# Performance work log

Hardware: AMD Instinct MI355X
Metric: run time of the kernel (lower is better)

The kernel has to match this reference:

```python
import jax, jax.numpy as jnp
import numpy as np

D_MODEL = 1024
NUM_PROTOTYPES = 1024
TOPK = 5
ALPHA = 0.1
EPS = 1e-12  # matches torch F.normalize default eps


def setup_inputs() -> dict:
    key = jax.random.key(0)
    kx, kp = jax.random.split(key)
    x = jax.random.normal(kx, (32, 2048, D_MODEL), dtype=jnp.float32)
    prototypes = jax.random.normal(kp, (NUM_PROTOTYPES, D_MODEL), dtype=jnp.float32)
    return {"x": x, "prototypes": prototypes}


def _l2_normalize(v, axis=-1):
    # torch F.normalize: v / max(||v||, eps)
    n = jnp.linalg.norm(v, axis=axis, keepdims=True)
    return v / jnp.maximum(n, EPS)


def reference(x, prototypes):
    # x: [B, L, D]; prototypes: [P, D]
    query = jnp.mean(x, axis=1)                       # [B, D] global pool
    query_n = _l2_normalize(query)                    # [B, D]
    proto_n = _l2_normalize(prototypes)               # [P, D]
    scores = jnp.einsum('bd,pd->bp', query_n, proto_n)  # [B, P] cosine sims
    topk_scores, topk_idx = jax.lax.top_k(scores, TOPK)  # [B, K]
    attn = jax.nn.softmax(topk_scores, axis=-1)       # [B, K]
    retrieved = prototypes[topk_idx]                  # [B, K, D] gather
    proto_agg = jnp.einsum('bk,bkd->bd', attn, retrieved)  # [B, D]
    out = x + ALPHA * proto_agg[:, None, :]           # broadcast residual add
    return out
```

## Files before the change

### kernel.cpp

```cpp
#include <hip/hip_runtime.h>
#include <math.h>

#define D_MODEL 1024
#define D4 256
#define SEQ 2048
#define BATCH 32
#define NUM_PROTO 1024
#define TOPK 5
#define ALPHA 0.1f
#define EPS 1e-12f
#define CHUNKS 64
#define CHUNK_ROWS (SEQ / CHUNKS)

typedef float f4v __attribute__((ext_vector_type(4)));

__device__ __forceinline__ float block_reduce_sum_256(float v) {
    __shared__ float red[4];
    for (int o = 32; o; o >>= 1) v += __shfl_down(v, o, 64);
    const int wave = threadIdx.x >> 6;
    const int lane = threadIdx.x & 63;
    __syncthreads();
    if (lane == 0) red[wave] = v;
    __syncthreads();
    return (red[0] + red[1]) + (red[2] + red[3]);
}

__global__ void mean_partial(const float* __restrict__ x, float* __restrict__ part) {
    const int blk = blockIdx.x;
    const int b = blk >> 6;
    const int c = blk & (CHUNKS - 1);
    const int t = threadIdx.x;
    const float4* xb = (const float4*)(x + (size_t)b * SEQ * D_MODEL
                                         + (size_t)c * CHUNK_ROWS * D_MODEL);
    float4 acc = {0.f, 0.f, 0.f, 0.f};
#pragma unroll 8
    for (int l = 0; l < CHUNK_ROWS; ++l) {
        float4 v = xb[(size_t)l * D4 + t];
        acc.x += v.x; acc.y += v.y; acc.z += v.z; acc.w += v.w;
    }
    ((float4*)part)[(size_t)blk * D4 + t] = acc;
}

__global__ void mean_finish(const float* __restrict__ part, float* __restrict__ qn) {
    const int b = blockIdx.x;
    const int t = threadIdx.x;
    float4 acc = {0.f, 0.f, 0.f, 0.f};
    for (int c = 0; c < CHUNKS; ++c) {
        float4 v = ((const float4*)part)[(size_t)(b * CHUNKS + c) * D4 + t];
        acc.x += v.x; acc.y += v.y; acc.z += v.z; acc.w += v.w;
    }
    const float s = 1.0f / (float)SEQ;
    acc.x *= s; acc.y *= s; acc.z *= s; acc.w *= s;
    const float qn2 = block_reduce_sum_256(acc.x * acc.x + acc.y * acc.y +
                                           acc.z * acc.z + acc.w * acc.w);
    const float inv = 1.0f / fmaxf(sqrtf(qn2), EPS);
    float4 o = {acc.x * inv, acc.y * inv, acc.z * inv, acc.w * inv};
    ((float4*)qn)[(size_t)b * D4 + t] = o;
}

__global__ void scores_kernel(const float* __restrict__ qn,
                              const float* __restrict__ proto,
                              float* __restrict__ scores) {
    const int p = blockIdx.x;
    const int t = threadIdx.x;
    const int wave = t >> 6, lane = t & 63;
    const float4 pv = ((const float4*)proto)[(size_t)p * D4 + t];
    const float pn2 = block_reduce_sum_256(pv.x * pv.x + pv.y * pv.y +
                                           pv.z * pv.z + pv.w * pv.w);
    const float inv_pn = 1.0f / fmaxf(sqrtf(pn2), EPS);

    __shared__ float ps[BATCH][4];
    for (int b = 0; b < BATCH; ++b) {
        const float4 q = ((const float4*)qn)[(size_t)b * D4 + t];
        float d = q.x * pv.x + q.y * pv.y + q.z * pv.z + q.w * pv.w;
        for (int o = 32; o; o >>= 1) d += __shfl_down(d, o, 64);
        if (lane == 0) ps[b][wave] = d;
    }
    __syncthreads();
    if (t < BATCH) {
        const float s = (ps[t][0] + ps[t][1]) + (ps[t][2] + ps[t][3]);
        scores[(size_t)t * NUM_PROTO + p] = s * inv_pn;
    }
}

__global__ void topk_agg(const float* __restrict__ scores,
                         const float* __restrict__ proto,
                         float* __restrict__ agg) {
    const int b = blockIdx.x;
    const int t = threadIdx.x;

    __shared__ float sc[NUM_PROTO];
    for (int i = t; i < NUM_PROTO; i += 256)
        sc[i] = scores[(size_t)b * NUM_PROTO + i];
    __syncthreads();

    __shared__ float topv[TOPK];
    __shared__ int   topi[TOPK];
    __shared__ float rv[4];
    __shared__ int   ri[4];

    for (int k = 0; k < TOPK; ++k) {
        float bv = -INFINITY;
        int   bi = 0x7fffffff;
        for (int i = t; i < NUM_PROTO; i += 256) {
            const float v = sc[i];
            if (v > bv) { bv = v; bi = i; }
        }
        for (int o = 32; o; o >>= 1) {
            const float ov = __shfl_down(bv, o, 64);
            const int   oi = __shfl_down(bi, o, 64);
            if (ov > bv || (ov == bv && oi < bi)) { bv = ov; bi = oi; }
        }
        const int wave = t >> 6, lane = t & 63;
        __syncthreads();
        if (lane == 0) { rv[wave] = bv; ri[wave] = bi; }
        __syncthreads();
        if (t == 0) {
            float fv = rv[0]; int fi = ri[0];
            for (int w = 1; w < 4; ++w)
                if (rv[w] > fv || (rv[w] == fv && ri[w] < fi)) { fv = rv[w]; fi = ri[w]; }
            topv[k] = fv;
            topi[k] = fi;
            sc[fi] = -INFINITY;
        }
        __syncthreads();
    }

    const float m = topv[0];
    float e[TOPK], s = 0.f;
    for (int k = 0; k < TOPK; ++k) { e[k] = expf(topv[k] - m); s += e[k]; }
    const float inv_s = 1.0f / s;

    float4 acc = {0.f, 0.f, 0.f, 0.f};
    for (int k = 0; k < TOPK; ++k) {
        const float a = e[k] * inv_s;
        const float4 pv = ((const float4*)proto)[(size_t)topi[k] * D4 + t];
        acc.x += a * pv.x; acc.y += a * pv.y; acc.z += a * pv.z; acc.w += a * pv.w;
    }
    ((float4*)agg)[(size_t)b * D4 + t] = acc;
}

__global__ void residual_add(const float* __restrict__ x,
                             const float* __restrict__ agg,
                             float* __restrict__ out) {
    const int blk = blockIdx.x;
    const int b   = blk >> 8;
    const int seg = blk & 255;
    const int t = threadIdx.x;
    const size_t base = ((size_t)b * SEQ + (size_t)seg * 8) * D4 + t;

    const float4 av = ((const float4*)agg)[(size_t)b * D4 + t];
    const float ax = ALPHA * av.x, ay = ALPHA * av.y,
                az = ALPHA * av.z, aw = ALPHA * av.w;

    const f4v* x4 = (const f4v*)x;
    f4v* out4 = (f4v*)out;
#pragma unroll
    for (int r = 0; r < 8; ++r) {
        const size_t i = base + (size_t)r * D4;
        f4v xv = x4[i];
        f4v o;
        o.x = xv.x + ax; o.y = xv.y + ay; o.z = xv.z + az; o.w = xv.w + aw;
        __builtin_nontemporal_store(o, &out4[i]);
    }
}

extern "C" void kernel_launch(void* const* d_in, const int* in_sizes, int n_in,
                              void* d_out, int out_size, void* d_ws, size_t ws_size,
                              hipStream_t stream) {
    const float* x     = (const float*)d_in[0];
    const float* proto = (const float*)d_in[1];
    float* out = (float*)d_out;

    float* ws      = (float*)d_ws;
    float* part    = ws;
    float* qn      = part + (size_t)BATCH * CHUNKS * D_MODEL;
    float* scores  = qn + (size_t)BATCH * D_MODEL;
    float* agg     = scores + (size_t)BATCH * NUM_PROTO;

    mean_partial<<<BATCH * CHUNKS, 256, 0, stream>>>(x, part);
    mean_finish<<<BATCH, 256, 0, stream>>>(part, qn);
    scores_kernel<<<NUM_PROTO, 256, 0, stream>>>(qn, proto, scores);
    topk_agg<<<BATCH, 256, 0, stream>>>(scores, proto, agg);
    residual_add<<<8192, 256, 0, stream>>>(x, agg, out);
}
```

Baseline: 155.4 us.

## Fuse cosine-score computation into top-k aggregation kernel per batch

Removes the separate scores kernel and computes cosine similarities inside the per-batch top-k kernel, with each wave scanning a quarter of the prototypes and recomputing prototype norms. This drops one launch and the scores round-trip through global memory. In exchange, only 32 blocks run, and each re-reads the whole prototype matrix and recomputes norms, which reduces parallelism and adds redundant traffic.

```diff
diff --git a/kernel.cpp b/kernel.cpp
--- a/kernel.cpp
+++ b/kernel.cpp
@@ -58,40 +58,37 @@
     ((float4*)qn)[(size_t)b * D4 + t] = o;
 }
 
-__global__ void scores_kernel(const float* __restrict__ qn,
-                              const float* __restrict__ proto,
-                              float* __restrict__ scores) {
-    const int p = blockIdx.x;
+__global__ void scores_topk_agg(const float* __restrict__ qn,
+                                const float* __restrict__ proto,
+                                float* __restrict__ agg) {
+    const int b = blockIdx.x;
     const int t = threadIdx.x;
     const int wave = t >> 6, lane = t & 63;
-    const float4 pv = ((const float4*)proto)[(size_t)p * D4 + t];
-    const float pn2 = block_reduce_sum_256(pv.x * pv.x + pv.y * pv.y +
-                                           pv.z * pv.z + pv.w * pv.w);
-    const float inv_pn = 1.0f / fmaxf(sqrtf(pn2), EPS);
 
-    __shared__ float ps[BATCH][4];
-    for (int b = 0; b < BATCH; ++b) {
-        const float4 q = ((const float4*)qn)[(size_t)b * D4 + t];
-        float d = q.x * pv.x + q.y * pv.y + q.z * pv.z + q.w * pv.w;
-        for (int o = 32; o; o >>= 1) d += __shfl_down(d, o, 64);
-        if (lane == 0) ps[b][wave] = d;
-    }
-    __syncthreads();
-    if (t < BATCH) {
-        const float s = (ps[t][0] + ps[t][1]) + (ps[t][2] + ps[t][3]);
-        scores[(size_t)t * NUM_PROTO + p] = s * inv_pn;
-    }
-}
-
-__global__ void topk_agg(const float* __restrict__ scores,
-                         const float* __restrict__ proto,
-                         float* __restrict__ agg) {
-    const int b = blockIdx.x;
-    const int t = threadIdx.x;
+    const float4* qb = (const float4*)(qn + (size_t)b * D_MODEL) + lane * 4;
+    const float4 q0 = qb[0], q1 = qb[1], q2 = qb[2], q3 = qb[3];
 
     __shared__ float sc[NUM_PROTO];
-    for (int i = t; i < NUM_PROTO; i += 256)
-        sc[i] = scores[(size_t)b * NUM_PROTO + i];
+
+    const int pbase = wave * (NUM_PROTO / 4);
+    for (int pp = 0; pp < NUM_PROTO / 4; ++pp) {
+        const int p = pbase + pp;
+        const float4* pr = (const float4*)(proto + (size_t)p * D_MODEL) + lane * 4;
+        const float4 p0 = pr[0], p1 = pr[1], p2 = pr[2], p3 = pr[3];
+        float d = q0.x * p0.x + q0.y * p0.y + q0.z * p0.z + q0.w * p0.w
+                + q1.x * p1.x + q1.y * p1.y + q1.z * p1.z + q1.w * p1.w
+                + q2.x * p2.x + q2.y * p2.y + q2.z * p2.z + q2.w * p2.w
+                + q3.x * p3.x + q3.y * p3.y + q3.z * p3.z + q3.w * p3.w;
+        float n = p0.x * p0.x + p0.y * p0.y + p0.z * p0.z + p0.w * p0.w
+                + p1.x * p1.x + p1.y * p1.y + p1.z * p1.z + p1.w * p1.w
+                + p2.x * p2.x + p2.y * p2.y + p2.z * p2.z + p2.w * p2.w
+                + p3.x * p3.x + p3.y * p3.y + p3.z * p3.z + p3.w * p3.w;
+        for (int o = 32; o; o >>= 1) {
+            d += __shfl_down(d, o, 64);
+            n += __shfl_down(n, o, 64);
+        }
+        if (lane == 0) sc[p] = d / fmaxf(sqrtf(n), EPS);
+    }
     __syncthreads();
 
     __shared__ float topv[TOPK];
@@ -111,7 +108,6 @@
             const int   oi = __shfl_down(bi, o, 64);
             if (ov > bv || (ov == bv && oi < bi)) { bv = ov; bi = oi; }
         }
-        const int wave = t >> 6, lane = t & 63;
         __syncthreads();
         if (lane == 0) { rv[wave] = bv; ri[wave] = bi; }
         __syncthreads();
@@ -175,12 +171,10 @@
     float* ws      = (float*)d_ws;
     float* part    = ws;
     float* qn      = part + (size_t)BATCH * CHUNKS * D_MODEL;
-    float* scores  = qn + (size_t)BATCH * D_MODEL;
-    float* agg     = scores + (size_t)BATCH * NUM_PROTO;
+    float* agg     = qn + (size_t)BATCH * D_MODEL;
 
     mean_partial<<<BATCH * CHUNKS, 256, 0, stream>>>(x, part);
     mean_finish<<<BATCH, 256, 0, stream>>>(part, qn);
-    scores_kernel<<<NUM_PROTO, 256, 0, stream>>>(qn, proto, scores);
-    topk_agg<<<BATCH, 256, 0, stream>>>(scores, proto, agg);
+    scores_topk_agg<<<BATCH, 256, 0, stream>>>(qn, proto, agg);
     residual_add<<<8192, 256, 0, stream>>>(x, agg, out);
 }
```

New measurement: 343.5 us. 2.21x slower.
